# Optimization experiments

Measured on AMD Instinct MI355X. Metric: run time of the kernel, lower is better.

Reference implementation:

```python
import jax, jax.numpy as jnp
import numpy as np

B, N, C_IN, G = 8, 65536, 16, 64
CH = [16, 16]
EPS = 1e-3  # keras BatchNormalization default epsilon
OFFSETS = [(dx, dy, dz) for dx in (-1, 0, 1) for dy in (-1, 0, 1) for dz in (-1, 0, 1)]
G3 = G * G * G


def setup_inputs() -> dict:
    key = jax.random.key(0)
    k = jax.random.split(key, 8)
    voxel_features = jax.random.normal(k[0], (B, N, C_IN), dtype=jnp.float32)
    # unique active voxel coordinates per example (submanifold sites)
    lin = jax.vmap(lambda kk: jax.random.permutation(kk, G3)[:N])(jax.random.split(k[1], B))
    xyz = jnp.stack([lin // (G * G), (lin // G) % G, lin % G], axis=-1).astype(jnp.int32)
    num_valid_voxels = jax.random.randint(k[2], (B,), N // 2, N + 1).astype(jnp.int32)
    w0 = jax.random.uniform(k[3], (3, 3, 3, C_IN, CH[0]), minval=-0.05, maxval=0.05, dtype=jnp.float32)
    w1 = jax.random.uniform(k[4], (3, 3, 3, CH[0], CH[1]), minval=-0.05, maxval=0.05, dtype=jnp.float32)
    nw0 = jax.random.uniform(k[5], (3, 3, 3, 1, 1), minval=-0.05, maxval=0.05, dtype=jnp.float32)
    nw1 = jax.random.uniform(k[6], (3, 3, 3, 1, 1), minval=-0.05, maxval=0.05, dtype=jnp.float32)
    gamma0 = jnp.ones((CH[0],), jnp.float32); beta0 = jnp.zeros((CH[0],), jnp.float32)
    gamma1 = jnp.ones((CH[1],), jnp.float32); beta1 = jnp.zeros((CH[1],), jnp.float32)
    return dict(voxel_features=voxel_features, voxel_xyz_indices=xyz,
                num_valid_voxels=num_valid_voxels, w0=w0, w1=w1, nw0=nw0, nw1=nw1,
                gamma0=gamma0, beta0=beta0, gamma1=gamma1, beta1=beta1)


def build_neighbor_idx(coords, valid_mask):
    """For each voxel and each 3x3x3 offset, the row index of the active neighbor, or -1."""
    lin = coords[..., 0] * (G * G) + coords[..., 1] * G + coords[..., 2]  # [B,N]
    # invalid (padded) voxels write to a spare slot so they never match as neighbors
    write_lin = jnp.where(valid_mask, lin, G3 + 1)
    idx_map = jnp.full((B, G3 + 2), -1, jnp.int32)
    idx_map = idx_map.at[jnp.arange(B)[:, None], write_lin].set(
        jnp.broadcast_to(jnp.arange(N, dtype=jnp.int32)[None, :], (B, N)))
    brow = jnp.arange(B)[:, None]
    nb = []
    for dx, dy, dz in OFFSETS:
        nx = coords[..., 0] + dx; ny = coords[..., 1] + dy; nz = coords[..., 2] + dz
        inb = (nx >= 0) & (nx < G) & (ny >= 0) & (ny < G) & (nz >= 0) & (nz < G)
        nlin = jnp.where(inb, nx * (G * G) + ny * G + nz, G3)  # slot G3 always -1
        nb.append(idx_map[brow, nlin])
    return jnp.stack(nb, axis=1)  # [B,27,N]


def sparse_conv(feats, nb_idx, valid_mask, w):
    """Submanifold sparse 3D conv: output only at active sites, gathering active neighbors."""
    wf = w.reshape(27, w.shape[3], w.shape[4])  # offsets enumerate kernel taps in order
    out = jnp.zeros((feats.shape[0], feats.shape[1], w.shape[4]), feats.dtype)
    for o in range(27):
        idx = nb_idx[:, o]  # [B,N]
        g = jnp.take_along_axis(feats, jnp.maximum(idx, 0)[..., None], axis=1)
        g = jnp.where((idx >= 0)[..., None], g, 0.0)
        out = out + jnp.einsum('bnc,co->bno', g, wf[o])
    return out * valid_mask[..., None]


def masked_bn(x, valid_mask, num_valid, gamma, beta):
    m = valid_mask[..., None].astype(x.dtype)
    cnt = jnp.sum(num_valid).astype(x.dtype)
    mean = jnp.sum(x * m, axis=(0, 1)) / cnt
    var = jnp.sum(m * jnp.square(x - mean), axis=(0, 1)) / cnt
    xn = (x - mean) * jax.lax.rsqrt(var + EPS) * gamma + beta
    return xn * m  # padded rows are zero-padded, as in the TF layer


def reference(voxel_features, voxel_xyz_indices, num_valid_voxels,
              w0, w1, nw0, nw1, gamma0, beta0, gamma1, beta1):
    valid_mask = jnp.arange(N)[None, :] < num_valid_voxels[:, None]  # [B,N]
    nb_idx = build_neighbor_idx(voxel_xyz_indices, valid_mask)
    ones = jnp.ones((B, N, 1), jnp.float32)
    net = voxel_features
    for w, nw, g, b in ((w0, nw0, gamma0, beta0), (w1, nw1, gamma1, beta1)):
        net = sparse_conv(net, nb_idx, valid_mask, w)
        net_norm = sparse_conv(ones, nb_idx, valid_mask, nw)
        net = net / (1.0 + jnp.abs(net_norm))
        net = masked_bn(net, valid_mask, num_valid_voxels, g, b)
        net = jax.nn.relu(net)
    return net
```

## Files before the change

kernel.cpp:

```cpp
#include <hip/hip_runtime.h>
#include <cstdint>
#include <cstddef>

#define NB 8
#define NN 65536
#define NS (NN + 16)
#define GG 64
#define GG3 (GG*GG*GG)
#define NW (GG3/32)
#define NBLKC 2048
#define EPSC 1e-3f

typedef __bf16 bf16x8 __attribute__((ext_vector_type(8)));
typedef float  f32x4  __attribute__((ext_vector_type(4)));

__device__ __forceinline__ unsigned short f2bf(float f) {
    unsigned u = __builtin_bit_cast(unsigned, f);
    unsigned r = (u + 0x7fffu + ((u >> 16) & 1u)) >> 16;
    return (unsigned short)r;
}
__device__ __forceinline__ unsigned pk2(float a, float b) {
    return (unsigned)f2bf(a) | ((unsigned)f2bf(b) << 16);
}
__device__ __forceinline__ float bf2f(unsigned short s) {
    return __builtin_bit_cast(float, (unsigned)s << 16);
}

__device__ __forceinline__ int site_rank2(const int2* __restrict__ mwb, int lin) {
    int2 mw = mwb[lin >> 5];
    uint32_t w = (uint32_t)mw.x;
    uint32_t bit = 1u << (lin & 31);
    if (!(w & bit)) return -1;
    return mw.y + __popc(w & (bit - 1u));
}

__global__ __launch_bounds__(256) void build_mask_kernel(
    const int* __restrict__ xyz, const int* __restrict__ nvv,
    uint32_t* __restrict__ mask,
    const float* __restrict__ w0, const float* __restrict__ w1,
    unsigned short* __restrict__ wf)
{
    int b = blockIdx.y;
    int n = blockIdx.x * 256 + threadIdx.x;
    if (n < nvv[b]) {
        const int* cp = xyz + ((size_t)b * NN + n) * 3;
        int lin = cp[0] * (GG * GG) + cp[1] * GG + cp[2];
        atomicOr(&mask[b * NW + (lin >> 5)], 1u << (lin & 31));
    }
    if (blockIdx.x == 0 && b < 2) {
        const float* w = b ? w1 : w0;
        unsigned short* o = wf + b * 14 * 512;
        for (int idx = threadIdx.x; idx < 14 * 512; idx += 256) {
            int i = idx >> 9;
            int rem = idx & 511;
            int L = rem >> 3, j = rem & 7;
            int quad = L >> 4, nn = L & 15;
            int off = 2 * i + (quad >> 1);
            int c = ((quad & 1) << 3) + j;
            float v = (off < 27) ? w[(off * 16 + c) * 16 + nn] : 0.f;
            o[idx] = f2bf(v);
        }
    }
}

__global__ __launch_bounds__(256) void scan_mask_kernel(
    const uint32_t* __restrict__ mask, int2* __restrict__ mwb)
{
    int b = blockIdx.x;
    const uint32_t* mb = mask + (size_t)b * NW;
    int2* wb = mwb + (size_t)b * NW;
    int t = threadIdx.x;

    uint32_t wv[32];
    int cnts[32];
    int local = 0;
    #pragma unroll
    for (int i = 0; i < 32; i++) {
        wv[i] = mb[t * 32 + i];
        cnts[i] = __popc(wv[i]);
        local += cnts[i];
    }

    __shared__ int sc[256];
    sc[t] = local;
    __syncthreads();
    for (int off = 1; off < 256; off <<= 1) {
        int v = (t >= off) ? sc[t - off] : 0;
        __syncthreads();
        sc[t] += v;
        __syncthreads();
    }
    int base = sc[t] - local;
    #pragma unroll
    for (int i = 0; i < 32; i++) {
        wb[t * 32 + i] = make_int2((int)wv[i], base);
        base += cnts[i];
    }
}

__global__ __launch_bounds__(256) void perm_gather_kernel(
    const int* __restrict__ xyz, const int* __restrict__ nvv,
    const int2* __restrict__ mwb,
    const float* __restrict__ feats,
    int2* __restrict__ srow,
    unsigned short* __restrict__ sfeats,
    int* __restrict__ rinv)
{
    int b = blockIdx.y;
    int n = blockIdx.x * 256 + threadIdx.x;
    int cnt = nvv[b];
    unsigned short* sfb = sfeats + (size_t)b * NS * 16;
    if (blockIdx.x == 0 && threadIdx.x < 16)
        sfb[(size_t)NN * 16 + threadIdx.x] = 0;
    if (n < cnt) {
        const int* cp = xyz + ((size_t)b * NN + n) * 3;
        int lin = cp[0] * (GG * GG) + cp[1] * GG + cp[2];
        int r = site_rank2(mwb + (size_t)b * NW, lin);
        srow[(size_t)b * NN + r] = make_int2(lin, n);
        rinv[(size_t)b * NN + n] = r;
        const float4* fp = (const float4*)(feats + ((size_t)b * NN + n) * 16);
        float4 f0 = fp[0], f1 = fp[1], f2 = fp[2], f3 = fp[3];
        uint4 lo = make_uint4(pk2(f0.x, f0.y), pk2(f0.z, f0.w),
                              pk2(f1.x, f1.y), pk2(f1.z, f1.w));
        uint4 hi = make_uint4(pk2(f2.x, f2.y), pk2(f2.z, f2.w),
                              pk2(f3.x, f3.y), pk2(f3.z, f3.w));
        *(uint4*)(sfb + (size_t)r * 16)     = lo;
        *(uint4*)(sfb + (size_t)r * 16 + 8) = hi;
    } else {
        uint4 z = make_uint4(0, 0, 0, 0);
        *(uint4*)(sfb + (size_t)n * 16)     = z;
        *(uint4*)(sfb + (size_t)n * 16 + 8) = z;
    }
}

__global__ __launch_bounds__(256, 4) void conv_mfma_kernel(
    const unsigned short* __restrict__ sfeats,
    const int2*     __restrict__ srow,
    const int*      __restrict__ nvv,
    const int2*     __restrict__ mwb,
    const unsigned short* __restrict__ wfrag,
    const float*    __restrict__ nw,
    unsigned short* __restrict__ outbuf,
    float*          __restrict__ stats)
{
    int lane = threadIdx.x & 63;
    int wv = threadIdx.x >> 6;
    int m = lane & 15, quad = lane >> 4;
    int v = lane & 31, h = lane >> 5;

    int b    = blockIdx.x & 7;
    int widb = (blockIdx.x >> 3) * 4 + wv;

    __shared__ int   jj[4][32][29];
    __shared__ float rrl[4][32];
    __shared__ float red[4][32];
    __shared__ float lnw[27];

    if (threadIdx.x < 27) lnw[threadIdx.x] = nw[threadIdx.x];

    bf16x8 bfr[14];
    #pragma unroll
    for (int i = 0; i < 14; i++)
        bfr[i] = *(const bf16x8*)(wfrag + i * 512 + lane * 8);
    __syncthreads();

    float psum = 0.f, psq = 0.f;
    int coff = (quad & 1) << 3;

    int cnt = nvv[b];
    const int2* mb = mwb + (size_t)b * NW;
    const unsigned short* fb = sfeats + (size_t)b * NS * 16;
    const int2* sr = srow + (size_t)b * NN;

    #pragma unroll 1
    for (int k = 0; k < 2; k++) {
        int r0 = (widb + k * 1024) << 5;
        if (r0 >= cnt) continue;

        int Rv = r0 + v;
        bool vld = Rv < cnt;
        int lin = vld ? sr[Rv].x : 0;
        int x = lin >> 12, y = (lin >> 6) & 63, z = lin & 63;
        int zb = z & 31;
        float nc = 0.f;
        #pragma unroll
        for (int t = 0; t < 5; t++) {
            int c = 2 * t + h;
            bool cok = c < 9;
            int cc = cok ? c : 0;
            int dx = cc / 3 - 1, dy = cc % 3 - 1;
            int nx = x + dx, ny = y + dy;
            bool colok = cok & ((unsigned)nx < 64u) & ((unsigned)ny < 64u);
            int wdi = colok ? (((nx << 12) + (ny << 6) + z) >> 5) : 0;

            int2 mw = make_int2(0, 0);
            if (vld & colok) mw = mb[wdi];
            bool need2 = vld & colok & (((zb == 0) & (z > 0)) | ((zb == 31) & (z < 63)));
            int w2 = wdi + ((zb == 0) ? -1 : 1);
            int2 mw2 = make_int2(0, 0);
            if (need2) mw2 = mb[w2];

            #pragma unroll
            for (int dz = -1; dz <= 1; dz++) {
                int zz = z + dz;
                bool zok = (unsigned)zz < 64u;
                bool same = (dz == 0) | ((dz < 0) ? (zb != 0) : (zb != 31));
                int2 word = same ? mw : mw2;
                int bb = zz & 31;
                uint32_t wm = (uint32_t)word.x;
                bool hit = vld & colok & zok & ((wm >> bb) & 1u);
                int rnk = word.y + __popc(wm & ((1u << bb) - 1u));
                int off = cc * 3 + dz + 1;
                int jv = hit ? rnk : NN;
                if (cok) {
                    jj[wv][v][off] = jv;
                    nc += hit ? lnw[off] : 0.f;
                }
            }
        }
        nc += __shfl_xor(nc, 32, 64);
        if (lane < 32) rrl[wv][v] = 1.f / (1.f + fabsf(nc));

        f32x4 acc0 = {0.f, 0.f, 0.f, 0.f};
        f32x4 acc1 = {0.f, 0.f, 0.f, 0.f};
        #pragma unroll
        for (int i = 0; i < 14; i++) {
            int off = 2 * i + (quad >> 1);
            int idx = off < 27 ? off : 28;
            int j0 = jj[wv][m][idx];      j0 = (off < 27) ? j0 : NN;
            int j1 = jj[wv][m + 16][idx]; j1 = (off < 27) ? j1 : NN;
            bf16x8 a0 = *(const bf16x8*)(fb + (size_t)j0 * 16 + coff);
            bf16x8 a1 = *(const bf16x8*)(fb + (size_t)j1 * 16 + coff);
            acc0 = __builtin_amdgcn_mfma_f32_16x16x32_bf16(a0, bfr[i], acc0, 0, 0, 0);
            acc1 = __builtin_amdgcn_mfma_f32_16x16x32_bf16(a1, bfr[i], acc1, 0, 0, 0);
        }

        #pragma unroll
        for (int hh = 0; hh < 2; hh++) {
            int rbase = r0 + (hh << 4);
            #pragma unroll
            for (int r4 = 0; r4 < 4; r4++) {
                int row = (quad << 2) + r4;
                float tval = (hh ? acc1[r4] : acc0[r4]) * rrl[wv][(hh << 4) + row];
                psum += tval; psq += tval * tval;
                int Rr = rbase + row;
                if (Rr < cnt)
                    outbuf[((size_t)b * NN + Rr) * 16 + m] = f2bf(tval);
            }
        }
    }

    psum += __shfl_xor(psum, 16, 64); psum += __shfl_xor(psum, 32, 64);
    psq  += __shfl_xor(psq, 16, 64);  psq  += __shfl_xor(psq, 32, 64);
    if (lane < 16) { red[wv][lane] = psum; red[wv][16 + lane] = psq; }
    __syncthreads();
    if (threadIdx.x < 32) {
        float vv = red[0][threadIdx.x] + red[1][threadIdx.x] +
                   red[2][threadIdx.x] + red[3][threadIdx.x];
        atomicAdd(&stats[(blockIdx.x & 15) * 32 + threadIdx.x], vv);
    }
}

__device__ __forceinline__ void compute_sb(
    const float* __restrict__ stats, const int* __restrict__ nvv,
    const float* __restrict__ gamma, const float* __restrict__ beta,
    float* sbs , float* sums )
{
    int tid = threadIdx.x;
    if (tid < 32) {
        float v = 0.f;
        #pragma unroll
        for (int s = 0; s < 16; s++) v += stats[s * 32 + tid];
        sums[tid] = v;
    }
    __syncthreads();
    if (tid < 16) {
        float cnt = 0.f;
        #pragma unroll
        for (int b = 0; b < NB; b++) cnt += (float)nvv[b];
        float mean = sums[tid] / cnt;
        float var  = fmaxf(sums[16 + tid] / cnt - mean * mean, 0.f);
        float scv = gamma[tid] * rsqrtf(var + EPSC);
        sbs[tid]      = scv;
        sbs[16 + tid] = beta[tid] - mean * scv;
    }
    __syncthreads();
}

__global__ __launch_bounds__(256) void bnrelu_sorted_kernel(
    const unsigned short* __restrict__ in, const float* __restrict__ stats,
    const int* __restrict__ nvv,
    const float* __restrict__ gamma, const float* __restrict__ beta,
    unsigned short* __restrict__ outb)
{
    __shared__ float sbs[32];
    __shared__ float sums[32];
    compute_sb(stats, nvv, gamma, beta, sbs, sums);

    int b = blockIdx.y;
    int r = blockIdx.x * 256 + threadIdx.x;
    if (r > NN) return;
    int cnt = nvv[b];
    uint4 lo = make_uint4(0, 0, 0, 0), hi = lo;
    if (r < cnt) {
        const uint4* ip = (const uint4*)(in + ((size_t)b * NN + r) * 16);
        uint4 xl = ip[0], xh = ip[1];
        float y[16];
        #pragma unroll
        for (int c = 0; c < 16; c++) {
            unsigned u = (c < 8) ? ((const unsigned*)&xl)[c >> 1]
                                 : ((const unsigned*)&xh)[(c - 8) >> 1];
            unsigned short sv = (c & 1) ? (unsigned short)(u >> 16)
                                        : (unsigned short)(u & 0xffff);
            y[c] = fmaxf(fmaf(bf2f(sv), sbs[c], sbs[16 + c]), 0.f);
        }
        lo = make_uint4(pk2(y[0], y[1]), pk2(y[2], y[3]), pk2(y[4], y[5]), pk2(y[6], y[7]));
        hi = make_uint4(pk2(y[8], y[9]), pk2(y[10], y[11]), pk2(y[12], y[13]), pk2(y[14], y[15]));
    }
    unsigned short* op = outb + ((size_t)b * NS + r) * 16;
    *(uint4*)op       = lo;
    *(uint4*)(op + 8) = hi;
}

__global__ __launch_bounds__(256) void final_out_kernel(
    const unsigned short* __restrict__ in,
    const int* __restrict__ rinv,
    const float* __restrict__ stats, const int* __restrict__ nvv,
    const float* __restrict__ gamma, const float* __restrict__ beta,
    float* __restrict__ out)
{
    __shared__ float sbs[32];
    __shared__ float sums[32];
    compute_sb(stats, nvv, gamma, beta, sbs, sums);

    int b = blockIdx.y;
    int n = blockIdx.x * 256 + threadIdx.x;
    int cnt = nvv[b];
    float4* op = (float4*)(out + ((size_t)b * NN + n) * 16);
    if (n < cnt) {
        int r = rinv[(size_t)b * NN + n];
        const uint4* ip = (const uint4*)(in + ((size_t)b * NN + r) * 16);
        uint4 xl = ip[0], xh = ip[1];
        float y[16];
        #pragma unroll
        for (int c = 0; c < 16; c++) {
            unsigned u = (c < 8) ? ((const unsigned*)&xl)[c >> 1]
                                 : ((const unsigned*)&xh)[(c - 8) >> 1];
            unsigned short sv = (c & 1) ? (unsigned short)(u >> 16)
                                        : (unsigned short)(u & 0xffff);
            y[c] = fmaxf(fmaf(bf2f(sv), sbs[c], sbs[16 + c]), 0.f);
        }
        op[0] = make_float4(y[0],  y[1],  y[2],  y[3]);
        op[1] = make_float4(y[4],  y[5],  y[6],  y[7]);
        op[2] = make_float4(y[8],  y[9],  y[10], y[11]);
        op[3] = make_float4(y[12], y[13], y[14], y[15]);
    } else {
        float4 z = make_float4(0.f, 0.f, 0.f, 0.f);
        op[0] = z; op[1] = z; op[2] = z; op[3] = z;
    }
}

extern "C" void kernel_launch(void* const* d_in, const int* in_sizes, int n_in,
                              void* d_out, int out_size, void* d_ws, size_t ws_size,
                              hipStream_t stream)
{
    const float* feats  = (const float*)d_in[0];
    const int*   xyz    = (const int*)d_in[1];
    const int*   nvv    = (const int*)d_in[2];
    const float* w0     = (const float*)d_in[3];
    const float* w1     = (const float*)d_in[4];
    const float* nw0    = (const float*)d_in[5];
    const float* nw1    = (const float*)d_in[6];
    const float* gamma0 = (const float*)d_in[7];
    const float* beta0  = (const float*)d_in[8];
    const float* gamma1 = (const float*)d_in[9];
    const float* beta1  = (const float*)d_in[10];
    float* out = (float*)d_out;

    char* ws = (char*)d_ws;
    uint32_t* mask    = (uint32_t*)ws;       ws += (size_t)NB * NW * 4;
    float*    stats1  = (float*)ws;          ws += 16 * 32 * 4;
    float*    stats2  = (float*)ws;          ws += 16 * 32 * 4;
    int2*     mwb     = (int2*)ws;           ws += (size_t)NB * NW * 8;
    int2*     srow    = (int2*)ws;           ws += (size_t)NB * NN * 8;
    unsigned short* sfA = (unsigned short*)ws; ws += (size_t)NB * NS * 16 * 2;
    unsigned short* sfB = (unsigned short*)ws; ws += (size_t)NB * NS * 16 * 2;
    unsigned short* bufPre = (unsigned short*)ws; ws += (size_t)NB * NN * 16 * 2;
    unsigned short* wfr = (unsigned short*)ws; ws += (size_t)2 * 14 * 512 * 2;
    int*      rinv    = (int*)ws;            ws += (size_t)NB * NN * 4;

    hipMemsetAsync(mask, 0, (size_t)NB * NW * 4 + 16 * 32 * 4 * 2, stream);

    dim3 gridBN(NN / 256, NB);
    build_mask_kernel<<<gridBN, 256, 0, stream>>>(xyz, nvv, mask, w0, w1, wfr);
    scan_mask_kernel<<<NB, 256, 0, stream>>>(mask, mwb);
    perm_gather_kernel<<<gridBN, 256, 0, stream>>>(xyz, nvv, mwb, feats, srow, sfA, rinv);

    conv_mfma_kernel<<<NBLKC, 256, 0, stream>>>(
        sfA, srow, nvv, mwb, wfr, nw0, bufPre, stats1);
    bnrelu_sorted_kernel<<<dim3(NN / 256 + 1, NB), 256, 0, stream>>>(
        bufPre, stats1, nvv, gamma0, beta0, sfB);

    conv_mfma_kernel<<<NBLKC, 256, 0, stream>>>(
        sfB, srow, nvv, mwb, wfr + 14 * 512, nw1, bufPre, stats2);

    final_out_kernel<<<dim3(NN / 256, NB), 256, 0, stream>>>(
        bufPre, rinv, stats2, nvv, gamma1, beta1, out);
}
```

Before: 236.3 us.

## Fuse mask build and scan into one LDS kernel; use nontemporal stores

```diff
diff --git a/kernel.cpp b/kernel.cpp
--- a/kernel.cpp
+++ b/kernel.cpp
@@ -13,6 +13,7 @@
 
 typedef __bf16 bf16x8 __attribute__((ext_vector_type(8)));
 typedef float  f32x4  __attribute__((ext_vector_type(4)));
+typedef unsigned uint32x4 __attribute__((ext_vector_type(4)));
 
 __device__ __forceinline__ unsigned short f2bf(float f) {
     unsigned u = __builtin_bit_cast(unsigned, f);
@@ -34,23 +35,63 @@
     return mw.y + __popc(w & (bit - 1u));
 }
 
-__global__ __launch_bounds__(256) void build_mask_kernel(
+__global__ __launch_bounds__(1024) void mask_scan_kernel(
     const int* __restrict__ xyz, const int* __restrict__ nvv,
-    uint32_t* __restrict__ mask,
+    int2* __restrict__ mwb,
     const float* __restrict__ w0, const float* __restrict__ w1,
-    unsigned short* __restrict__ wf)
-{
-    int b = blockIdx.y;
-    int n = blockIdx.x * 256 + threadIdx.x;
-    if (n < nvv[b]) {
-        const int* cp = xyz + ((size_t)b * NN + n) * 3;
-        int lin = cp[0] * (GG * GG) + cp[1] * GG + cp[2];
-        atomicOr(&mask[b * NW + (lin >> 5)], 1u << (lin & 31));
-    }
-    if (blockIdx.x == 0 && b < 2) {
+    unsigned short* __restrict__ wf,
+    float* __restrict__ stats1, float* __restrict__ stats2)
+{
+    __shared__ uint32_t lmask[NW];
+    __shared__ int sc[1024];
+    int b = blockIdx.x;
+    int t = threadIdx.x;
+
+    #pragma unroll
+    for (int i = 0; i < NW / 1024; i++) lmask[t + i * 1024] = 0u;
+    if (b == 0 && t < 512) { stats1[t] = 0.f; stats2[t] = 0.f; }
+    __syncthreads();
+
+    int cnt = nvv[b];
+    #pragma unroll 4
+    for (int n = t; n < NN; n += 1024) {
+        if (n < cnt) {
+            const int* cp = xyz + ((size_t)b * NN + n) * 3;
+            int lin = cp[0] * (GG * GG) + cp[1] * GG + cp[2];
+            atomicOr(&lmask[lin >> 5], 1u << (lin & 31));
+        }
+    }
+    __syncthreads();
+
+    uint32_t wv[8];
+    int cnts[8];
+    int local = 0;
+    #pragma unroll
+    for (int i = 0; i < 8; i++) {
+        wv[i] = lmask[t * 8 + i];
+        cnts[i] = __popc(wv[i]);
+        local += cnts[i];
+    }
+    sc[t] = local;
+    __syncthreads();
+    for (int off = 1; off < 1024; off <<= 1) {
+        int v = (t >= off) ? sc[t - off] : 0;
+        __syncthreads();
+        sc[t] += v;
+        __syncthreads();
+    }
+    int base = sc[t] - local;
+    int2* wb = mwb + (size_t)b * NW;
+    #pragma unroll
+    for (int i = 0; i < 8; i++) {
+        wb[t * 8 + i] = make_int2((int)wv[i], base);
+        base += cnts[i];
+    }
+
+    if (b < 2) {
         const float* w = b ? w1 : w0;
         unsigned short* o = wf + b * 14 * 512;
-        for (int idx = threadIdx.x; idx < 14 * 512; idx += 256) {
+        for (int idx = t; idx < 14 * 512; idx += 1024) {
             int i = idx >> 9;
             int rem = idx & 511;
             int L = rem >> 3, j = rem & 7;
@@ -60,41 +101,6 @@
             float v = (off < 27) ? w[(off * 16 + c) * 16 + nn] : 0.f;
             o[idx] = f2bf(v);
         }
-    }
-}
-
-__global__ __launch_bounds__(256) void scan_mask_kernel(
-    const uint32_t* __restrict__ mask, int2* __restrict__ mwb)
-{
-    int b = blockIdx.x;
-    const uint32_t* mb = mask + (size_t)b * NW;
-    int2* wb = mwb + (size_t)b * NW;
-    int t = threadIdx.x;
-
-    uint32_t wv[32];
-    int cnts[32];
-    int local = 0;
-    #pragma unroll
-    for (int i = 0; i < 32; i++) {
-        wv[i] = mb[t * 32 + i];
-        cnts[i] = __popc(wv[i]);
-        local += cnts[i];
-    }
-
-    __shared__ int sc[256];
-    sc[t] = local;
-    __syncthreads();
-    for (int off = 1; off < 256; off <<= 1) {
-        int v = (t >= off) ? sc[t - off] : 0;
-        __syncthreads();
-        sc[t] += v;
-        __syncthreads();
-    }
-    int base = sc[t] - local;
-    #pragma unroll
-    for (int i = 0; i < 32; i++) {
-        wb[t * 32 + i] = make_int2((int)wv[i], base);
-        base += cnts[i];
     }
 }
 
@@ -120,16 +126,16 @@
         rinv[(size_t)b * NN + n] = r;
         const float4* fp = (const float4*)(feats + ((size_t)b * NN + n) * 16);
         float4 f0 = fp[0], f1 = fp[1], f2 = fp[2], f3 = fp[3];
-        uint4 lo = make_uint4(pk2(f0.x, f0.y), pk2(f0.z, f0.w),
-                              pk2(f1.x, f1.y), pk2(f1.z, f1.w));
-        uint4 hi = make_uint4(pk2(f2.x, f2.y), pk2(f2.z, f2.w),
-                              pk2(f3.x, f3.y), pk2(f3.z, f3.w));
-        *(uint4*)(sfb + (size_t)r * 16)     = lo;
-        *(uint4*)(sfb + (size_t)r * 16 + 8) = hi;
+        uint32x4 lo = { pk2(f0.x, f0.y), pk2(f0.z, f0.w),
+                        pk2(f1.x, f1.y), pk2(f1.z, f1.w) };
+        uint32x4 hi = { pk2(f2.x, f2.y), pk2(f2.z, f2.w),
+                        pk2(f3.x, f3.y), pk2(f3.z, f3.w) };
+        __builtin_nontemporal_store(lo, (uint32x4*)(sfb + (size_t)r * 16));
+        __builtin_nontemporal_store(hi, (uint32x4*)(sfb + (size_t)r * 16 + 8));
     } else {
-        uint4 z = make_uint4(0, 0, 0, 0);
-        *(uint4*)(sfb + (size_t)n * 16)     = z;
-        *(uint4*)(sfb + (size_t)n * 16 + 8) = z;
+        uint32x4 z = { 0u, 0u, 0u, 0u };
+        __builtin_nontemporal_store(z, (uint32x4*)(sfb + (size_t)n * 16));
+        __builtin_nontemporal_store(z, (uint32x4*)(sfb + (size_t)n * 16 + 8));
     }
 }
 
@@ -245,7 +251,8 @@
                 psum += tval; psq += tval * tval;
                 int Rr = rbase + row;
                 if (Rr < cnt)
-                    outbuf[((size_t)b * NN + Rr) * 16 + m] = f2bf(tval);
+                    __builtin_nontemporal_store(
+                        f2bf(tval), &outbuf[((size_t)b * NN + Rr) * 16 + m]);
             }
         }
     }
@@ -301,7 +308,7 @@
     int r = blockIdx.x * 256 + threadIdx.x;
     if (r > NN) return;
     int cnt = nvv[b];
-    uint4 lo = make_uint4(0, 0, 0, 0), hi = lo;
+    uint32x4 lo = { 0u, 0u, 0u, 0u }, hi = lo;
     if (r < cnt) {
         const uint4* ip = (const uint4*)(in + ((size_t)b * NN + r) * 16);
         uint4 xl = ip[0], xh = ip[1];
@@ -314,12 +321,14 @@
                                         : (unsigned short)(u & 0xffff);
             y[c] = fmaxf(fmaf(bf2f(sv), sbs[c], sbs[16 + c]), 0.f);
         }
-        lo = make_uint4(pk2(y[0], y[1]), pk2(y[2], y[3]), pk2(y[4], y[5]), pk2(y[6], y[7]));
-        hi = make_uint4(pk2(y[8], y[9]), pk2(y[10], y[11]), pk2(y[12], y[13]), pk2(y[14], y[15]));
+        lo = (uint32x4){ pk2(y[0], y[1]), pk2(y[2], y[3]),
+                         pk2(y[4], y[5]), pk2(y[6], y[7]) };
+        hi = (uint32x4){ pk2(y[8], y[9]), pk2(y[10], y[11]),
+                         pk2(y[12], y[13]), pk2(y[14], y[15]) };
     }
     unsigned short* op = outb + ((size_t)b * NS + r) * 16;
-    *(uint4*)op       = lo;
-    *(uint4*)(op + 8) = hi;
+    __builtin_nontemporal_store(lo, (uint32x4*)op);
+    __builtin_nontemporal_store(hi, (uint32x4*)(op + 8));
 }
 
 __global__ __launch_bounds__(256) void final_out_kernel(
@@ -336,7 +345,7 @@
     int b = blockIdx.y;
     int n = blockIdx.x * 256 + threadIdx.x;
     int cnt = nvv[b];
-    float4* op = (float4*)(out + ((size_t)b * NN + n) * 16);
+    f32x4* op = (f32x4*)(out + ((size_t)b * NN + n) * 16);
     if (n < cnt) {
         int r = rinv[(size_t)b * NN + n];
         const uint4* ip = (const uint4*)(in + ((size_t)b * NN + r) * 16);
@@ -350,13 +359,16 @@
                                         : (unsigned short)(u & 0xffff);
             y[c] = fmaxf(fmaf(bf2f(sv), sbs[c], sbs[16 + c]), 0.f);
         }
-        op[0] = make_float4(y[0],  y[1],  y[2],  y[3]);
-        op[1] = make_float4(y[4],  y[5],  y[6],  y[7]);
-        op[2] = make_float4(y[8],  y[9],  y[10], y[11]);
-        op[3] = make_float4(y[12], y[13], y[14], y[15]);
+        __builtin_nontemporal_store((f32x4){y[0],  y[1],  y[2],  y[3]},  op);
+        __builtin_nontemporal_store((f32x4){y[4],  y[5],  y[6],  y[7]},  op + 1);
+        __builtin_nontemporal_store((f32x4){y[8],  y[9],  y[10], y[11]}, op + 2);
+        __builtin_nontemporal_store((f32x4){y[12], y[13], y[14], y[15]}, op + 3);
     } else {
-        float4 z = make_float4(0.f, 0.f, 0.f, 0.f);
-        op[0] = z; op[1] = z; op[2] = z; op[3] = z;
+        f32x4 z = { 0.f, 0.f, 0.f, 0.f };
+        __builtin_nontemporal_store(z, op);
+        __builtin_nontemporal_store(z, op + 1);
+        __builtin_nontemporal_store(z, op + 2);
+        __builtin_nontemporal_store(z, op + 3);
     }
 }
 
@@ -378,7 +390,6 @@
     float* out = (float*)d_out;
 
     char* ws = (char*)d_ws;
-    uint32_t* mask    = (uint32_t*)ws;       ws += (size_t)NB * NW * 4;
     float*    stats1  = (float*)ws;          ws += 16 * 32 * 4;
     float*    stats2  = (float*)ws;          ws += 16 * 32 * 4;
     int2*     mwb     = (int2*)ws;           ws += (size_t)NB * NW * 8;
@@ -389,11 +400,10 @@
     unsigned short* wfr = (unsigned short*)ws; ws += (size_t)2 * 14 * 512 * 2;
     int*      rinv    = (int*)ws;            ws += (size_t)NB * NN * 4;
 
-    hipMemsetAsync(mask, 0, (size_t)NB * NW * 4 + 16 * 32 * 4 * 2, stream);
+    mask_scan_kernel<<<NB, 1024, 0, stream>>>(
+        xyz, nvv, mwb, w0, w1, wfr, stats1, stats2);
 
     dim3 gridBN(NN / 256, NB);
-    build_mask_kernel<<<gridBN, 256, 0, stream>>>(xyz, nvv, mask, w0, w1, wfr);
-    scan_mask_kernel<<<NB, 256, 0, stream>>>(mask, mwb);
     perm_gather_kernel<<<gridBN, 256, 0, stream>>>(xyz, nvv, mwb, feats, srow, sfA, rinv);
 
     conv_mfma_kernel<<<NBLKC, 256, 0, stream>>>(
```

New measurement: 257.4 us. 8.9% more time.
